# Performance work log

Measured on AMD Instinct MI355X. Metric: run time of the kernel, lower is better.

## Reference

```python
import jax, jax.numpy as jnp
import numpy as np

B, T, C, H = 4, 2048, 1024, 16

def setup_inputs() -> dict:
    key = jax.random.key(0)
    ks = jax.random.split(key, 5)
    s = 1.0 / np.sqrt(C)
    return {
        "x": jax.random.normal(ks[0], (B, T, C), jnp.float32),
        "Wq": jax.random.normal(ks[1], (C, C), jnp.float32) * s,
        "bq": jnp.zeros((C,), jnp.float32),
        "Wk": jax.random.normal(ks[2], (C, C), jnp.float32) * s,
        "bk": jnp.zeros((C,), jnp.float32),
        "Wv": jax.random.normal(ks[3], (C, C), jnp.float32) * s,
        "bv": jnp.zeros((C,), jnp.float32),
        "Wp": jax.random.normal(ks[4], (C, C), jnp.float32) * s,
        "bp": jnp.zeros((C,), jnp.float32),
    }

def reference(x, Wq, bq, Wk, bk, Wv, bv, Wp, bp):
    b, t, c = x.shape
    hd = c // H  # head dim
    # projections; W stored as [in, out] (torch Linear transposed)
    q = (x @ Wq + bq).reshape(b, t, H, hd).transpose(0, 2, 1, 3)  # [B,H,T,hd]
    k = (x @ Wk + bk).reshape(b, t, H, hd).transpose(0, 2, 1, 3)
    v = (x @ Wv + bv).reshape(b, t, H, hd).transpose(0, 2, 1, 3)
    att = jnp.einsum("bhqd,bhkd->bhqk", q, k) * (1.0 / np.sqrt(hd))
    causal = jnp.tril(jnp.ones((t, t), bool))
    att = jnp.where(causal, att, -jnp.inf)
    att = jax.nn.softmax(att, axis=-1)
    y = jnp.einsum("bhqk,bhkd->bhqd", att, v)  # [B,H,T,hd]
    y = y.transpose(0, 2, 1, 3).reshape(b, t, c)
    return y @ Wp + bp
```

## Files before the change

### kernel.cpp

```cpp
#include <hip/hip_runtime.h>
#include <stdint.h>

#define B_  4
#define T_  2048
#define C_  1024
#define H_  16
#define HD_ 64
#define M_  (B_*T_)

typedef __attribute__((ext_vector_type(8)))  __bf16 bf16x8;
typedef __attribute__((ext_vector_type(4)))  float  f32x4;
typedef __attribute__((ext_vector_type(16))) float  f32x16;
typedef __attribute__((ext_vector_type(4)))  unsigned int u32x4;

#define QSCALE 0.18033688011112042f
#define SMSHIFT 12.0f

__device__ __forceinline__ unsigned short f2bf(float f) {
    union { float f; unsigned int u; } v; v.f = f;
    unsigned int r = v.u + 0x7fffu + ((v.u >> 16) & 1u);
    return (unsigned short)(r >> 16);
}
__device__ __forceinline__ unsigned int pack2(float a, float b) {
    return (unsigned int)f2bf(a) | ((unsigned int)f2bf(b) << 16);
}
__device__ __forceinline__ void gload16(const void* g, void* l) {
    __builtin_amdgcn_global_load_lds(
        (const __attribute__((address_space(1))) unsigned int*)(uintptr_t)g,
        (__attribute__((address_space(3))) unsigned int*)(unsigned int)(uintptr_t)l,
        16, 0, 0);
}

__global__ __launch_bounds__(256) void k_cvt_x(const float* __restrict__ x,
                                               unsigned short* __restrict__ xb, int n8) {
    int i = blockIdx.x * blockDim.x + threadIdx.x;
    if (i >= n8) return;
    const float4* p = (const float4*)x + (size_t)i * 2;
    float4 a = p[0], b = p[1];
    u32x4 o = { pack2(a.x, a.y), pack2(a.z, a.w), pack2(b.x, b.y), pack2(b.z, b.w) };
    *(u32x4*)(xb + (size_t)i * 8) = o;
}

__global__ __launch_bounds__(256) void k_transpose4(
    const float* __restrict__ Wq, const float* __restrict__ Wk,
    const float* __restrict__ Wv, const float* __restrict__ Wp,
    unsigned short* __restrict__ wqkvt, unsigned short* __restrict__ wpt) {
    __shared__ float tile[32][33];
    int z = blockIdx.z;
    const float* src = (z == 0) ? Wq : (z == 1) ? Wk : (z == 2) ? Wv : Wp;
    unsigned short* dst = (z < 3) ? wqkvt + ((size_t)z << 20) : wpt;
    int c0 = blockIdx.x * 32, r0 = blockIdx.y * 32;
    int tx = threadIdx.x, ty = threadIdx.y;
    for (int i = 0; i < 4; i++)
        tile[ty + i * 8][tx] = src[(size_t)(r0 + ty + i * 8) * C_ + c0 + tx];
    __syncthreads();
    for (int i = 0; i < 4; i++)
        dst[(size_t)(c0 + ty + i * 8) * C_ + r0 + tx] = f2bf(tile[tx][ty + i * 8]);
}

__device__ __forceinline__ void g_stage(const unsigned short* __restrict__ A,
                                        const unsigned short* __restrict__ Bt,
                                        int m0, int n0, char* lds, int tid, int slot, int kt)
{
    char* base = lds + slot * 32768;
    #pragma unroll
    for (int j = 0; j < 4; j++) {
        int L = tid * 16 + j * 4096;
        int rr = L >> 7;
        int cc = ((((L & 127) >> 4) ^ (rr & 7)) << 3);
        gload16(A  + (size_t)(m0 + rr) * C_ + kt * 64 + cc, base + L);
        gload16(Bt + (size_t)(n0 + rr) * C_ + kt * 64 + cc, base + 16384 + L);
    }
}

template<int MODE>
__global__ __launch_bounds__(256, 2) void k_gemm(
    const unsigned short* __restrict__ A,
    const unsigned short* __restrict__ Bt,
    const float* __restrict__ bias0, const float* __restrict__ bias1,
    const float* __restrict__ bias2,
    unsigned short* __restrict__ qo, unsigned short* __restrict__ ko,
    unsigned short* __restrict__ vto, float* __restrict__ outf)
{
    __shared__ __align__(16) char lds[65536];
    int m0 = blockIdx.x * 128, n0 = blockIdx.y * 128;
    int tid = threadIdx.x, w = tid >> 6, l = tid & 63;
    int wm = w >> 1, wn = w & 1;
    int lg = l >> 4, lr = l & 15;

    f32x4 acc[4][4];
    #pragma unroll
    for (int i = 0; i < 4; i++)
        #pragma unroll
        for (int j = 0; j < 4; j++) acc[i][j] = (f32x4){0.f, 0.f, 0.f, 0.f};

    g_stage(A, Bt, m0, n0, lds, tid, 0, 0);

    for (int t = 0; t < 16; t++) {
        if (t < 15) {
            g_stage(A, Bt, m0, n0, lds, tid, (t + 1) & 1, t + 1);
            asm volatile("s_waitcnt vmcnt(8)" ::: "memory");
        } else {
            asm volatile("s_waitcnt vmcnt(0)" ::: "memory");
        }
        __builtin_amdgcn_s_barrier();
        __builtin_amdgcn_sched_barrier(0);
        const char* baseA = lds + (t & 1) * 32768;
        const char* baseB = baseA + 16384;
        #pragma unroll
        for (int ks = 0; ks < 2; ks++) {
            bf16x8 af[4], bfr[4];
            #pragma unroll
            for (int fi = 0; fi < 4; fi++) {
                int row = wm * 64 + fi * 16 + lr;
                af[fi] = *(const bf16x8*)(baseA + row * 128 + ((((ks << 2) | lg) ^ (row & 7)) << 4));
            }
            #pragma unroll
            for (int fj = 0; fj < 4; fj++) {
                int row = wn * 64 + fj * 16 + lr;
                bfr[fj] = *(const bf16x8*)(baseB + row * 128 + ((((ks << 2) | lg) ^ (row & 7)) << 4));
            }
            #pragma unroll
            for (int fi = 0; fi < 4; fi++)
                #pragma unroll
                for (int fj = 0; fj < 4; fj++)
                    acc[fi][fj] = __builtin_amdgcn_mfma_f32_16x16x32_bf16(af[fi], bfr[fj], acc[fi][fj], 0, 0, 0);
        }
        __builtin_amdgcn_s_barrier();
    }

    #pragma unroll
    for (int i = 0; i < 4; i++) {
        #pragma unroll
        for (int j = 0; j < 4; j++) {
            int mrow = m0 + wm * 64 + i * 16 + lg * 4;
            int ncol = n0 + wn * 64 + j * 16 + lr;
            if (MODE == 0) {
                int sel = ncol >> 10, nc = ncol & 1023;
                int hh = nc >> 6, dd = nc & 63;
                const float* bp = (sel == 0) ? bias0 : (sel == 1) ? bias1 : bias2;
                float bvv = bp[nc];
                #pragma unroll
                for (int r = 0; r < 4; r++) {
                    int mm = mrow + r;
                    int bb = mm >> 11, tt = mm & (T_ - 1);
                    float v = acc[i][j][r] + bvv;
                    if (sel == 0)      qo[((size_t)((bb * H_ + hh) * T_) + tt) * HD_ + dd] = f2bf(v * QSCALE);
                    else if (sel == 1) ko[((size_t)((bb * H_ + hh) * T_) + tt) * HD_ + dd] = f2bf(v);
                    else               vto[((size_t)((bb * H_ + hh) * HD_) + dd) * T_ + tt] = f2bf(v);
                }
            } else {
                float bvv = bias0[ncol];
                #pragma unroll
                for (int r = 0; r < 4; r++)
                    outf[(size_t)(mrow + r) * C_ + ncol] = acc[i][j][r] + bvv;
            }
        }
    }
}

__device__ __forceinline__ void sm_pack(f32x16& st, bool mask, int lq, int lh,
                                        float& li, unsigned int* pw)
{
    if (mask) {
        #pragma unroll
        for (int r = 0; r < 16; r++) {
            int key = (r & 3) + 8 * (r >> 2) + 4 * lh;
            if (key > lq) st[r] = -1e30f;
        }
    }
    #pragma unroll
    for (int r = 0; r < 16; r++) st[r] = exp2f(st[r] - SMSHIFT);
    float rsum[8];
    #pragma unroll
    for (int i = 0; i < 8; i++) rsum[i] = st[2 * i] + st[2 * i + 1];
    #pragma unroll
    for (int i = 0; i < 4; i++) rsum[i] += rsum[i + 4];
    float rs = (rsum[0] + rsum[2]) + (rsum[1] + rsum[3]);
    rs += __shfl_xor(rs, 32);
    li += rs;
    #pragma unroll
    for (int kc = 0; kc < 2; kc++) {
        unsigned int a0, a1, b0, b1;
        asm("v_cvt_pk_bf16_f32 %0, %1, %2" : "=v"(a0) : "v"(st[kc*8+0]), "v"(st[kc*8+1]));
        asm("v_cvt_pk_bf16_f32 %0, %1, %2" : "=v"(a1) : "v"(st[kc*8+2]), "v"(st[kc*8+3]));
        asm("v_cvt_pk_bf16_f32 %0, %1, %2" : "=v"(b0) : "v"(st[kc*8+4]), "v"(st[kc*8+5]));
        asm("v_cvt_pk_bf16_f32 %0, %1, %2" : "=v"(b1) : "v"(st[kc*8+6]), "v"(st[kc*8+7]));
        asm volatile("v_permlane32_swap_b32 %0, %1" : "+v"(a0), "+v"(b0));
        asm volatile("v_permlane32_swap_b32 %0, %1" : "+v"(a1), "+v"(b1));
        pw[kc*4+0] = a0; pw[kc*4+1] = a1; pw[kc*4+2] = b0; pw[kc*4+3] = b1;
    }
}

__device__ __forceinline__ void pv_step(const unsigned int* pw, const bf16x8* vc,
                                        f32x16& o0, f32x16& o1)
{
    #pragma unroll
    for (int kc = 0; kc < 2; kc++) {
        union { u32x4 u; bf16x8 v; } pb;
        pb.u = (u32x4){pw[kc*4+0], pw[kc*4+1], pw[kc*4+2], pw[kc*4+3]};
        o0 = __builtin_amdgcn_mfma_f32_32x32x16_bf16(vc[kc*2],     pb.v, o0, 0, 0, 0);
        o1 = __builtin_amdgcn_mfma_f32_32x32x16_bf16(vc[kc*2 + 1], pb.v, o1, 0, 0, 0);
    }
}

__device__ __forceinline__ void attn_writeout(unsigned int (*otw)[36],
                                              const f32x16& o0, const f32x16& o1, float li,
                                              int lq, int lh, int l,
                                              unsigned short* dst)
{
    float inv = 1.f / li;
    #pragma unroll
    for (int r = 0; r < 16; r += 2) {
        int dh = ((r & 3) + 8 * (r >> 2) + 4 * lh) >> 1;
        otw[lq][dh]      = pack2(o0[r] * inv, o0[r + 1] * inv);
        otw[lq][16 + dh] = pack2(o1[r] * inv, o1[r + 1] * inv);
    }
    asm volatile("s_waitcnt lgkmcnt(0)" ::: "memory");
    __builtin_amdgcn_sched_barrier(0);
    #pragma unroll
    for (int i = 0; i < 4; i++) {
        int c = i * 64 + l;
        int q = c >> 3, ch = c & 7;
        u32x4 rv = *(const u32x4*)(&otw[q][ch * 4]);
        *(u32x4*)(dst + (size_t)q * C_ + ch * 8) = rv;
    }
}

__device__ __forceinline__ void stage_kv(const unsigned short* kp, const unsigned short* vp,
                                         char* ldsp, int kt, int tid)
{
    int r = tid >> 3, sl = tid & 7;
    #pragma unroll
    for (int c = 0; c < 2; c++) {
        int row = c * 32 + r;
        gload16(kp + ((size_t)(kt * 64 + row)) * HD_ + ((sl ^ (row & 7)) * 8),
                ldsp + c * 4096 + tid * 16);
    }
    #pragma unroll
    for (int c = 0; c < 2; c++) {
        int d = c * 32 + r;
        gload16(vp + (size_t)d * T_ + kt * 64 + ((sl ^ (d & 7)) * 8),
                ldsp + 8192 + c * 4096 + tid * 16);
    }
}

__global__ __launch_bounds__(256, 2) void k_attn(
    const unsigned short* __restrict__ qb,
    const unsigned short* __restrict__ kb,
    const unsigned short* __restrict__ vtb,
    unsigned short* __restrict__ yb)
{
    __shared__ __align__(16) char smem[32768];
    int bh = blockIdx.x;
    int x  = blockIdx.y;
    int h = bh & (H_ - 1), b = bh >> 4;
    int tid = threadIdx.x, w = tid >> 6, l = tid & 63;
    int lq = l & 31, lh = l >> 5;
    int p = x * 4 + w;
    int qtA = p, qtB = 63 - p;
    int qbA = qtA * 32, qbB = qtB * 32;
    int nt = 32 - 2 * x;

    const unsigned short* qp = qb  + (size_t)bh * T_ * HD_;
    const unsigned short* kp = kb  + (size_t)bh * T_ * HD_;
    const unsigned short* vp = vtb + (size_t)bh * HD_ * T_;

    bf16x8 qA[4], qB[4];
    #pragma unroll
    for (int dc = 0; dc < 4; dc++) {
        qA[dc] = *(const bf16x8*)(qp + (size_t)(qbA + lq) * HD_ + dc * 16 + lh * 8);
        qB[dc] = *(const bf16x8*)(qp + (size_t)(qbB + lq) * HD_ + dc * 16 + lh * 8);
    }

    f32x16 oA0, oA1, oB0, oB1;
    #pragma unroll
    for (int r = 0; r < 16; r++) { oA0[r] = 0.f; oA1[r] = 0.f; oB0[r] = 0.f; oB1[r] = 0.f; }
    float liA = 0.f, liB = 0.f;

    stage_kv(kp, vp, smem,         0, tid);
    stage_kv(kp, vp, smem + 16384, 1, tid);

    for (int t = 0; t < nt; t++) {
        if (t < nt - 1) asm volatile("s_waitcnt vmcnt(4)" ::: "memory");
        else            asm volatile("s_waitcnt vmcnt(0)" ::: "memory");
        __builtin_amdgcn_s_barrier();
        __builtin_amdgcn_sched_barrier(0);
        const unsigned short* Kb = (const unsigned short*)(smem + (t & 1) * 16384);
        const unsigned short* Vb = Kb + 4096;

        #pragma unroll
        for (int s = 0; s < 2; s++) {
            int kt32 = 2 * t + s;
            if (kt32 > qtB) break;
            bool doA = (kt32 <= qtA);

            bf16x8 kc[4], vc[4];
            #pragma unroll
            for (int dc = 0; dc < 4; dc++) {
                int row = s * 32 + lq;
                kc[dc] = *(const bf16x8*)(Kb + row * 64 + (((dc * 2 + lh) ^ (row & 7)) * 8));
            }
            #pragma unroll
            for (int vi = 0; vi < 4; vi++) {
                int d = lq + (vi & 1) * 32;
                int slot = (s * 4 + (vi >> 1) * 2 + lh) ^ (d & 7);
                vc[vi] = *(const bf16x8*)(Vb + d * 64 + slot * 8);
            }

            f32x16 stA, stB;
            #pragma unroll
            for (int r = 0; r < 16; r++) { stA[r] = 0.f; stB[r] = 0.f; }
            __builtin_amdgcn_s_setprio(1);
            #pragma unroll
            for (int dc = 0; dc < 4; dc++) {
                stB = __builtin_amdgcn_mfma_f32_32x32x16_bf16(kc[dc], qB[dc], stB, 0, 0, 0);
                if (doA)
                    stA = __builtin_amdgcn_mfma_f32_32x32x16_bf16(kc[dc], qA[dc], stA, 0, 0, 0);
            }
            __builtin_amdgcn_s_setprio(0);

            unsigned int pwA[8], pwB[8];
            sm_pack(stB, (kt32 == qtB), lq, lh, liB, pwB);
            if (doA) sm_pack(stA, (kt32 == qtA), lq, lh, liA, pwA);
            __builtin_amdgcn_s_setprio(1);
            pv_step(pwB, vc, oB0, oB1);
            if (doA) pv_step(pwA, vc, oA0, oA1);
            __builtin_amdgcn_s_setprio(0);
        }

        __builtin_amdgcn_s_barrier();
        __builtin_amdgcn_sched_barrier(0);
        if (t + 2 < nt) stage_kv(kp, vp, smem + (t & 1) * 16384, t + 2, tid);
    }

    unsigned int (*otw)[36] = (unsigned int (*)[36])(smem + w * 4608);
    unsigned short* dstA = yb + (size_t)(b * T_ + qbA) * C_ + h * HD_;
    unsigned short* dstB = yb + (size_t)(b * T_ + qbB) * C_ + h * HD_;
    attn_writeout(otw, oA0, oA1, liA, lq, lh, l, dstA);
    attn_writeout(otw, oB0, oB1, liB, lq, lh, l, dstB);
}

extern "C" void kernel_launch(void* const* d_in, const int* in_sizes, int n_in,
                              void* d_out, int out_size, void* d_ws, size_t ws_size,
                              hipStream_t stream) {
    const float* x  = (const float*)d_in[0];
    const float* Wq = (const float*)d_in[1];
    const float* bq = (const float*)d_in[2];
    const float* Wk = (const float*)d_in[3];
    const float* bk = (const float*)d_in[4];
    const float* Wv = (const float*)d_in[5];
    const float* bv = (const float*)d_in[6];
    const float* Wp = (const float*)d_in[7];
    const float* bp = (const float*)d_in[8];
    float* out = (float*)d_out;

    char* ws = (char*)d_ws;
    unsigned short* xb    = (unsigned short*)(ws);
    unsigned short* wqkvt = (unsigned short*)(ws + (16u << 20));
    unsigned short* wpt   = (unsigned short*)(ws + (22u << 20));
    unsigned short* qbuf  = (unsigned short*)(ws + (24u << 20));
    unsigned short* kbuf  = (unsigned short*)(ws + (40u << 20));
    unsigned short* vtbuf = (unsigned short*)(ws + (56u << 20));
    unsigned short* ybuf  = (unsigned short*)(ws + (72u << 20));

    int n8 = M_ * C_ / 8;
    k_cvt_x<<<(n8 + 255) / 256, 256, 0, stream>>>(x, xb, n8);

    k_transpose4<<<dim3(32, 32, 4), dim3(32, 8), 0, stream>>>(Wq, Wk, Wv, Wp, wqkvt, wpt);

    k_gemm<0><<<dim3(M_ / 128, 3 * C_ / 128), 256, 0, stream>>>(
        xb, wqkvt, bq, bk, bv, qbuf, kbuf, vtbuf, nullptr);

    k_attn<<<dim3(64, 8), 256, 0, stream>>>(qbuf, kbuf, vtbuf, ybuf);

    k_gemm<1><<<dim3(M_ / 128, C_ / 128), 256, 0, stream>>>(
        ybuf, wpt, bp, nullptr, nullptr, nullptr, nullptr, nullptr, out);
}
```

Measured before the change: 260.6 us.

## Split attention key sub-tiles across two wave groups and fuse prep kernels

The attention kernel now runs 512 threads per block. Two groups of four waves each handle one 32-key half of every 64-key tile, instead of one wave walking both halves in sequence. After the loop, partial outputs and row sums are merged through LDS, and each group writes out one of the two query tiles. K and V staging is split between the groups. Separately, the x conversion and the weight transposes are fused into one launch to save a kernel launch. This doubles the waves available to hide latency, at the cost of extra LDS, more barriers in the merge, and higher register pressure under the new launch bounds.

```diff
diff --git a/kernel.cpp b/kernel.cpp
--- a/kernel.cpp
+++ b/kernel.cpp
@@ -31,26 +31,31 @@
         16, 0, 0);
 }
 
-__global__ __launch_bounds__(256) void k_cvt_x(const float* __restrict__ x,
-                                               unsigned short* __restrict__ xb, int n8) {
-    int i = blockIdx.x * blockDim.x + threadIdx.x;
-    if (i >= n8) return;
-    const float4* p = (const float4*)x + (size_t)i * 2;
-    float4 a = p[0], b = p[1];
-    u32x4 o = { pack2(a.x, a.y), pack2(a.z, a.w), pack2(b.x, b.y), pack2(b.z, b.w) };
-    *(u32x4*)(xb + (size_t)i * 8) = o;
-}
-
-__global__ __launch_bounds__(256) void k_transpose4(
+__global__ __launch_bounds__(256) void k_prep(
+    const float* __restrict__ x,
     const float* __restrict__ Wq, const float* __restrict__ Wk,
     const float* __restrict__ Wv, const float* __restrict__ Wp,
+    unsigned short* __restrict__ xb,
     unsigned short* __restrict__ wqkvt, unsigned short* __restrict__ wpt) {
     __shared__ float tile[32][33];
     int z = blockIdx.z;
+    int tx = threadIdx.x, ty = threadIdx.y;
+    if (z == 4) {
+        int blk = blockIdx.y * 32 + blockIdx.x;
+        int tid = ty * 32 + tx;
+        #pragma unroll
+        for (int it = 0; it < 4; it++) {
+            int i = blk * 1024 + it * 256 + tid;
+            const float4* pp = (const float4*)x + (size_t)i * 2;
+            float4 a = pp[0], c = pp[1];
+            u32x4 o = { pack2(a.x, a.y), pack2(a.z, a.w), pack2(c.x, c.y), pack2(c.z, c.w) };
+            *(u32x4*)(xb + (size_t)i * 8) = o;
+        }
+        return;
+    }
     const float* src = (z == 0) ? Wq : (z == 1) ? Wk : (z == 2) ? Wv : Wp;
     unsigned short* dst = (z < 3) ? wqkvt + ((size_t)z << 20) : wpt;
     int c0 = blockIdx.x * 32, r0 = blockIdx.y * 32;
-    int tx = threadIdx.x, ty = threadIdx.y;
     for (int i = 0; i < 4; i++)
         tile[ty + i * 8][tx] = src[(size_t)(r0 + ty + i * 8) * C_ + c0 + tx];
     __syncthreads();
@@ -227,37 +232,73 @@
     }
 }
 
+__device__ __forceinline__ void merge_write(char* reg, const f32x16& o0, const f32x16& o1,
+                                            float li, int l)
+{
+    #pragma unroll
+    for (int j = 0; j < 4; j++)
+        *(f32x4*)(reg + l * 128 + ((j ^ (l & 7)) << 4)) =
+            (f32x4){o0[4*j], o0[4*j+1], o0[4*j+2], o0[4*j+3]};
+    #pragma unroll
+    for (int j = 0; j < 4; j++)
+        *(f32x4*)(reg + l * 128 + (((4 + j) ^ (l & 7)) << 4)) =
+            (f32x4){o1[4*j], o1[4*j+1], o1[4*j+2], o1[4*j+3]};
+    *(float*)(reg + 8192 + l * 4) = li;
+}
+__device__ __forceinline__ void merge_add(const char* reg, f32x16& o0, f32x16& o1,
+                                          float& li, int l)
+{
+    #pragma unroll
+    for (int j = 0; j < 4; j++) {
+        f32x4 v = *(const f32x4*)(reg + l * 128 + ((j ^ (l & 7)) << 4));
+        o0[4*j] += v[0]; o0[4*j+1] += v[1]; o0[4*j+2] += v[2]; o0[4*j+3] += v[3];
+    }
+    #pragma unroll
+    for (int j = 0; j < 4; j++) {
+        f32x4 v = *(const f32x4*)(reg + l * 128 + (((4 + j) ^ (l & 7)) << 4));
+        o1[4*j] += v[0]; o1[4*j+1] += v[1]; o1[4*j+2] += v[2]; o1[4*j+3] += v[3];
+    }
+    li += *(const float*)(reg + 8192 + l * 4);
+}
+
 __device__ __forceinline__ void stage_kv(const unsigned short* kp, const unsigned short* vp,
                                          char* ldsp, int kt, int tid)
 {
-    int r = tid >> 3, sl = tid & 7;
-    #pragma unroll
-    for (int c = 0; c < 2; c++) {
-        int row = c * 32 + r;
-        gload16(kp + ((size_t)(kt * 64 + row)) * HD_ + ((sl ^ (row & 7)) * 8),
-                ldsp + c * 4096 + tid * 16);
-    }
-    #pragma unroll
-    for (int c = 0; c < 2; c++) {
-        int d = c * 32 + r;
-        gload16(vp + (size_t)d * T_ + kt * 64 + ((sl ^ (d & 7)) * 8),
-                ldsp + 8192 + c * 4096 + tid * 16);
-    }
-}
-
-__global__ __launch_bounds__(256, 2) void k_attn(
+    int g = tid >> 8;
+    int u = tid & 255;
+    int r = u >> 3, sl = u & 7;
+    if (g == 0) {
+        #pragma unroll
+        for (int c = 0; c < 2; c++) {
+            int row = c * 32 + r;
+            gload16(kp + ((size_t)(kt * 64 + row)) * HD_ + ((sl ^ (row & 7)) * 8),
+                    ldsp + c * 4096 + u * 16);
+        }
+    } else {
+        #pragma unroll
+        for (int c = 0; c < 2; c++) {
+            int d = c * 32 + r;
+            gload16(vp + (size_t)d * T_ + kt * 64 + ((sl ^ (d & 7)) * 8),
+                    ldsp + 8192 + c * 4096 + u * 16);
+        }
+    }
+}
+
+__global__ __launch_bounds__(512, 4) void k_attn(
     const unsigned short* __restrict__ qb,
     const unsigned short* __restrict__ kb,
     const unsigned short* __restrict__ vtb,
     unsigned short* __restrict__ yb)
 {
-    __shared__ __align__(16) char smem[32768];
+    __shared__ __align__(16) char smem[36864];
     int bh = blockIdx.x;
     int x  = blockIdx.y;
     int h = bh & (H_ - 1), b = bh >> 4;
     int tid = threadIdx.x, w = tid >> 6, l = tid & 63;
     int lq = l & 31, lh = l >> 5;
-    int p = x * 4 + w;
+    int wp = w & 3;
+    int sw = w >> 2;
+    int p = x * 4 + wp;
     int qtA = p, qtB = 63 - p;
     int qbA = qtA * 32, qbB = qtB * 32;
     int nt = 32 - 2 * x;
@@ -282,29 +323,26 @@
     stage_kv(kp, vp, smem + 16384, 1, tid);
 
     for (int t = 0; t < nt; t++) {
-        if (t < nt - 1) asm volatile("s_waitcnt vmcnt(4)" ::: "memory");
+        if (t < nt - 1) asm volatile("s_waitcnt vmcnt(2)" ::: "memory");
         else            asm volatile("s_waitcnt vmcnt(0)" ::: "memory");
         __builtin_amdgcn_s_barrier();
         __builtin_amdgcn_sched_barrier(0);
         const unsigned short* Kb = (const unsigned short*)(smem + (t & 1) * 16384);
         const unsigned short* Vb = Kb + 4096;
 
-        #pragma unroll
-        for (int s = 0; s < 2; s++) {
-            int kt32 = 2 * t + s;
-            if (kt32 > qtB) break;
+        int kt32 = 2 * t + sw;
+        if (kt32 <= qtB) {
             bool doA = (kt32 <= qtA);
-
             bf16x8 kc[4], vc[4];
             #pragma unroll
             for (int dc = 0; dc < 4; dc++) {
-                int row = s * 32 + lq;
+                int row = sw * 32 + lq;
                 kc[dc] = *(const bf16x8*)(Kb + row * 64 + (((dc * 2 + lh) ^ (row & 7)) * 8));
             }
             #pragma unroll
             for (int vi = 0; vi < 4; vi++) {
                 int d = lq + (vi & 1) * 32;
-                int slot = (s * 4 + (vi >> 1) * 2 + lh) ^ (d & 7);
+                int slot = (sw * 4 + (vi >> 1) * 2 + lh) ^ (d & 7);
                 vc[vi] = *(const bf16x8*)(Vb + d * 64 + slot * 8);
             }
 
@@ -334,11 +372,25 @@
         if (t + 2 < nt) stage_kv(kp, vp, smem + (t & 1) * 16384, t + 2, tid);
     }
 
-    unsigned int (*otw)[36] = (unsigned int (*)[36])(smem + w * 4608);
-    unsigned short* dstA = yb + (size_t)(b * T_ + qbA) * C_ + h * HD_;
-    unsigned short* dstB = yb + (size_t)(b * T_ + qbB) * C_ + h * HD_;
-    attn_writeout(otw, oA0, oA1, liA, lq, lh, l, dstA);
-    attn_writeout(otw, oB0, oB1, liB, lq, lh, l, dstB);
+    __syncthreads();
+    char* mb = smem + wp * 8448;
+    if (sw)  merge_write(mb, oA0, oA1, liA, l);
+    __syncthreads();
+    if (!sw) merge_add(mb, oA0, oA1, liA, l);
+    __syncthreads();
+    if (!sw) merge_write(mb, oB0, oB1, liB, l);
+    __syncthreads();
+    if (sw)  merge_add(mb, oB0, oB1, liB, l);
+    __syncthreads();
+
+    unsigned int (*otw)[36] = (unsigned int (*)[36])(smem + sw * 18432 + wp * 4608);
+    if (!sw) {
+        unsigned short* dstA = yb + (size_t)(b * T_ + qbA) * C_ + h * HD_;
+        attn_writeout(otw, oA0, oA1, liA, lq, lh, l, dstA);
+    } else {
+        unsigned short* dstB = yb + (size_t)(b * T_ + qbB) * C_ + h * HD_;
+        attn_writeout(otw, oB0, oB1, liB, lq, lh, l, dstB);
+    }
 }
 
 extern "C" void kernel_launch(void* const* d_in, const int* in_sizes, int n_in,
@@ -364,15 +416,12 @@
     unsigned short* vtbuf = (unsigned short*)(ws + (56u << 20));
     unsigned short* ybuf  = (unsigned short*)(ws + (72u << 20));
 
-    int n8 = M_ * C_ / 8;
-    k_cvt_x<<<(n8 + 255) / 256, 256, 0, stream>>>(x, xb, n8);
-
-    k_transpose4<<<dim3(32, 32, 4), dim3(32, 8), 0, stream>>>(Wq, Wk, Wv, Wp, wqkvt, wpt);
+    k_prep<<<dim3(32, 32, 5), dim3(32, 8), 0, stream>>>(x, Wq, Wk, Wv, Wp, xb, wqkvt, wpt);
 
     k_gemm<0><<<dim3(M_ / 128, 3 * C_ / 128), 256, 0, stream>>>(
         xb, wqkvt, bq, bk, bv, qbuf, kbuf, vtbuf, nullptr);
 
-    k_attn<<<dim3(64, 8), 256, 0, stream>>>(qbuf, kbuf, vtbuf, ybuf);
+    k_attn<<<dim3(64, 8), 512, 0, stream>>>(qbuf, kbuf, vtbuf, ybuf);
 
     k_gemm<1><<<dim3(M_ / 128, C_ / 128), 256, 0, stream>>>(
         ybuf, wpt, bp, nullptr, nullptr, nullptr, nullptr, nullptr, out);
```

Measured after the change: 401.9 us. +54.2%, slower.
